# Kernel tuning notes

Hardware: AMD Instinct MI355X
Metric: run time of the kernel (lower is better)

Reference implementation:

```python
import jax, jax.numpy as jnp
import numpy as np
import math

B, S, HID = 1, 2048, 4096
HQ, HKV, D = 32, 8, 128
G = HQ // HKV          # GQA group size
OBS, W, SINK = 128, 32, 2
THETA = 500000.0
TOP_FRAC, MID_SPARSITY, LOW_FRAC = 0.05, 0.7, 0.20
K_KEEP = int(math.ceil((1.0 - MID_SPARSITY) * D))  # elements kept per level-1 token


def _rope(x):
    # x: [B, H, S, D]; standard Llama rotary embedding
    half = D // 2
    inv_freq = 1.0 / (THETA ** (jnp.arange(half, dtype=jnp.float32) / half))
    ang = jnp.arange(S, dtype=jnp.float32)[:, None] * inv_freq[None, :]  # [S, half]
    cos = jnp.concatenate([jnp.cos(ang), jnp.cos(ang)], axis=-1)  # [S, D]
    sin = jnp.concatenate([jnp.sin(ang), jnp.sin(ang)], axis=-1)
    x1, x2 = x[..., :half], x[..., half:]
    rot = jnp.concatenate([-x2, x1], axis=-1)
    return x * cos[None, None] + rot * sin[None, None]


def _topk_mask(x):
    # keep the K_KEEP largest-magnitude elements of each length-D token vector
    a = jnp.abs(x)
    thr = jnp.sort(a, axis=-1)[..., D - K_KEEP]
    return a >= thr[..., None]


def setup_inputs() -> dict:
    key = jax.random.key(0)
    ks = jax.random.split(key, 5)
    sc = HID ** -0.5
    return {
        "hidden_states": jax.random.normal(ks[0], (B, S, HID), dtype=jnp.float32),
        "wq": jax.random.normal(ks[1], (HID, HQ * D), dtype=jnp.float32) * sc,
        "wk": jax.random.normal(ks[2], (HID, HKV * D), dtype=jnp.float32) * sc,
        "wv": jax.random.normal(ks[3], (HID, HKV * D), dtype=jnp.float32) * sc,
        "wo": jax.random.normal(ks[4], (HQ * D, HID), dtype=jnp.float32) * sc,
    }


def reference(hidden_states, wq, wk, wv, wo):
    scale = 1.0 / math.sqrt(D)
    q = (hidden_states @ wq).reshape(B, S, HQ, D).transpose(0, 2, 1, 3)   # [B,HQ,S,D]
    k = (hidden_states @ wk).reshape(B, S, HKV, D).transpose(0, 2, 1, 3)  # [B,HKV,S,D]
    v = (hidden_states @ wv).reshape(B, S, HKV, D).transpose(0, 2, 1, 3)
    q, k = _rope(q), _rope(k)

    # --- observation-window GQA attention (grouped queries vs all keys) ---
    obs_q = q[:, :, S - OBS:, :].reshape(B, HKV, G, OBS, D)
    s_obs = jnp.einsum('bhgqd,bhkd->bhgqk', obs_q, k) * scale
    obs_causal = jnp.arange(S)[None, :] <= (S - OBS + jnp.arange(OBS))[:, None]  # [OBS,S]
    s_obs = jnp.where(obs_causal[None, None, None], s_obs, -jnp.inf)
    aw_kv = jax.nn.softmax(s_obs.astype(jnp.float32), axis=-1).mean(axis=2)  # [B,HKV,OBS,S]

    # per-token importance, normalized by how many obs queries observed each key
    counts = jnp.minimum(OBS, S - jnp.arange(S)).astype(jnp.float32)
    imp = aw_kv.sum(axis=2) / counts[None, None, :]  # [B,HKV,S]

    # --- global thresholds over the compressible region -> 3 sparsity levels ---
    imp_c = imp[:, :, :S - W].reshape(-1)
    t_high = jnp.quantile(imp_c, 1.0 - TOP_FRAC)
    t_low = jnp.quantile(imp_c, LOW_FRAC)
    level = jnp.where(imp >= t_high, 0, jnp.where(imp < t_low, 2, 1))
    pos = jnp.arange(S)
    dense_pos = (pos >= S - W) | (pos < SINK)     # recent window + sinks stay dense
    level = jnp.where(dense_pos[None, None, :], 0, level)

    keep_k = jnp.where((level == 0)[..., None], True, (level == 1)[..., None] & _topk_mask(k))
    keep_v = jnp.where((level == 0)[..., None], True, (level == 1)[..., None] & _topk_mask(v))
    k_sp = k * keep_k
    v_sp = v * keep_v
    evicted = level == 2

    # --- causal GQA attention over the sparsified KV cache ---
    q_g = q.reshape(B, HKV, G, S, D)
    s = jnp.einsum('bhgqd,bhkd->bhgqk', q_g, k_sp) * scale
    causal = jnp.tril(jnp.ones((S, S), dtype=bool))
    allow = causal[None, None, None] & (~evicted)[:, :, None, None, :]
    s = jnp.where(allow, s, -jnp.inf)
    p = jax.nn.softmax(s.astype(jnp.float32), axis=-1).astype(v_sp.dtype)
    o = jnp.einsum('bhgqk,bhkd->bhgqd', p, v_sp)
    o = o.reshape(B, HQ, S, D).transpose(0, 2, 1, 3).reshape(B, S, HQ * D)
    return o @ wo
```

## Files before the change

kernel.cpp:

```cpp
#include <hip/hip_runtime.h>
#include <hip/hip_bf16.h>
#include <math.h>

#define S_    2048
#define HID_  4096
#define HQ_   32
#define HKV_  8
#define D_    128
#define G_    4
#define OBS_  128
#define W_    32
#define NKV_  1024
#define NQ_   4096
#define KLD_  2048
#define SCALE_ 0.08838834764831845f
#define THR_IDX_ 89
#define NC_   16128

typedef __attribute__((ext_vector_type(4))) float f32x4;
typedef __attribute__((ext_vector_type(8))) short s16x8;
typedef __attribute__((ext_vector_type(8))) unsigned short u16x8;
typedef __attribute__((ext_vector_type(4))) unsigned short u16x4;
typedef unsigned short ushort_t;

struct TermPtrs { const ushort_t* a[6]; const ushort_t* b[6]; };
struct Six { const ushort_t* A[3]; const ushort_t* B[3]; };

__device__ __forceinline__ unsigned short f2bf(float x) {
  union { float f; unsigned u; } v; v.f = x;
  unsigned r = v.u + 0x7FFFu + ((v.u >> 16) & 1u);
  return (unsigned short)(r >> 16);
}
__device__ __forceinline__ float bf2f(unsigned short b) {
  union { unsigned u; float f; } v; v.u = ((unsigned)b) << 16;
  return v.f;
}
__device__ __forceinline__ void gload_lds16(const void* g, void* l) {
  __builtin_amdgcn_global_load_lds((const __attribute__((address_space(1))) unsigned int*)g,
                                   (__attribute__((address_space(3))) unsigned int*)l, 16, 0, 0);
}
__device__ __forceinline__ void term_sel(const TermPtrs& P, int tt,
                                         const ushort_t*& As, const ushort_t*& Bs) {
  switch (tt) {
    case 0: As = P.a[0]; Bs = P.b[0]; break;
    case 1: As = P.a[1]; Bs = P.b[1]; break;
    case 2: As = P.a[2]; Bs = P.b[2]; break;
    case 3: As = P.a[3]; Bs = P.b[3]; break;
    case 4: As = P.a[4]; Bs = P.b[4]; break;
    default: As = P.a[5]; Bs = P.b[5]; break;
  }
}
__device__ __forceinline__ void xcd_bmbn(int& bm, int& bn) {
  int nplane = gridDim.x * gridDim.y;
  int l = blockIdx.y * gridDim.x + blockIdx.x;
  int v = (l & 7) * (nplane >> 3) + (l >> 3);
  bm = v / gridDim.x;
  bn = v - bm * gridDim.x;
}

__global__ __launch_bounds__(256) void split3_kernel(const float* __restrict__ src,
                                                     ushort_t* __restrict__ d0,
                                                     ushort_t* __restrict__ d1,
                                                     ushort_t* __restrict__ d2, int n4) {
  int idx = blockIdx.x * 256 + threadIdx.x;
  if (idx >= n4) return;
  float4 v = ((const float4*)src)[idx];
  u16x4 o0, o1, o2;
  float xs[4] = {v.x, v.y, v.z, v.w};
#pragma unroll
  for (int e = 0; e < 4; ++e) {
    float x = xs[e];
    unsigned short b0 = f2bf(x);
    float r = x - bf2f(b0);
    unsigned short b1 = f2bf(r);
    o0[e] = b0; o1[e] = b1; o2[e] = f2bf(r - bf2f(b1));
  }
  *(u16x4*)(d0 + (size_t)idx * 4) = o0;
  *(u16x4*)(d1 + (size_t)idx * 4) = o1;
  *(u16x4*)(d2 + (size_t)idx * 4) = o2;
}

__global__ __launch_bounds__(256) void splitT_kernel(const float* __restrict__ src, int N,
                                                     ushort_t* __restrict__ t0,
                                                     ushort_t* __restrict__ t1,
                                                     ushort_t* __restrict__ t2) {
  __shared__ float tile[64][65];
  const int t = threadIdx.x;
  const int n0 = blockIdx.x * 64, k0 = blockIdx.y * 64;
#pragma unroll
  for (int i = 0; i < 16; ++i) {
    int idx = i * 256 + t;
    int r = idx >> 6, c = idx & 63;
    tile[r][c] = src[(size_t)(k0 + r) * N + n0 + c];
  }
  __syncthreads();
#pragma unroll
  for (int i = 0; i < 16; ++i) {
    int idx = i * 256 + t;
    int n = idx >> 6, kk = idx & 63;
    float x = tile[kk][n];
    unsigned short b0 = f2bf(x);
    size_t o = (size_t)(n0 + n) * HID_ + k0 + kk;
    t0[o] = b0;
    if (t1) {
      float r = x - bf2f(b0);
      unsigned short b1 = f2bf(r);
      t1[o] = b1;
      t2[o] = f2bf(r - bf2f(b1));
    }
  }
}

__global__ __launch_bounds__(256) void gemm6s(Six P, float* __restrict__ Cbase,
                                              int M, int N, int K, int KSTEPS) {
  __shared__ ushort_t lds[6 * 128 * 32];
  const int t = threadIdx.x;
  const int wave = t >> 6, lane = t & 63;
  const int lc = lane & 15, lg = lane >> 4;
  int bm, bn;
  xcd_bmbn(bm, bn);
  const int z = blockIdx.z;
  const int wm = wave >> 1, wn = wave & 1;
  float* C = Cbase + (size_t)z * M * N;

  f32x4 acc[4][4];
#pragma unroll
  for (int fi = 0; fi < 4; ++fi)
#pragma unroll
    for (int fj = 0; fj < 4; ++fj) acc[fi][fj] = 0.f;

  for (int kb = z * KSTEPS; kb < z * KSTEPS + KSTEPS; ++kb) {
    __syncthreads();
#pragma unroll
    for (int ti = 0; ti < 6; ++ti) {
      const ushort_t* src = (ti < 3) ? P.A[ti] : P.B[ti - 3];
      const int rb = ((ti < 3) ? bm : bn) * 128;
#pragma unroll
      for (int it = 0; it < 2; ++it) {
        int slot = it * 256 + t;
        int row = slot >> 2, cp = slot & 3;
        int c = (cp - (row >> 1)) & 3;
        gload_lds16(src + (size_t)(rb + row) * K + kb * 32 + c * 8,
                    lds + ti * 4096 + it * 2048 + wave * 512);
      }
    }
    __syncthreads();
    s16x8 a0[4], a1[4], a2[4], bfr[4];
#pragma unroll
    for (int f = 0; f < 4; ++f) {
      int ra = wm * 64 + f * 16 + lc;
      int ca = ((lg + (ra >> 1)) & 3) * 8;
      a0[f] = *(const s16x8*)(lds + 0 * 4096 + ra * 32 + ca);
      a1[f] = *(const s16x8*)(lds + 1 * 4096 + ra * 32 + ca);
      a2[f] = *(const s16x8*)(lds + 2 * 4096 + ra * 32 + ca);
    }
#pragma unroll
    for (int f = 0; f < 4; ++f) {
      int rb2 = wn * 64 + f * 16 + lc;
      bfr[f] = *(const s16x8*)(lds + 3 * 4096 + rb2 * 32 + (((lg + (rb2 >> 1)) & 3) * 8));
    }
#pragma unroll
    for (int fi = 0; fi < 4; ++fi)
#pragma unroll
      for (int fj = 0; fj < 4; ++fj) {
        acc[fi][fj] = __builtin_amdgcn_mfma_f32_16x16x32_bf16(a0[fi], bfr[fj], acc[fi][fj], 0, 0, 0);
        acc[fi][fj] = __builtin_amdgcn_mfma_f32_16x16x32_bf16(a1[fi], bfr[fj], acc[fi][fj], 0, 0, 0);
        acc[fi][fj] = __builtin_amdgcn_mfma_f32_16x16x32_bf16(a2[fi], bfr[fj], acc[fi][fj], 0, 0, 0);
      }
#pragma unroll
    for (int f = 0; f < 4; ++f) {
      int rb2 = wn * 64 + f * 16 + lc;
      bfr[f] = *(const s16x8*)(lds + 4 * 4096 + rb2 * 32 + (((lg + (rb2 >> 1)) & 3) * 8));
    }
#pragma unroll
    for (int fi = 0; fi < 4; ++fi)
#pragma unroll
      for (int fj = 0; fj < 4; ++fj) {
        acc[fi][fj] = __builtin_amdgcn_mfma_f32_16x16x32_bf16(a0[fi], bfr[fj], acc[fi][fj], 0, 0, 0);
        acc[fi][fj] = __builtin_amdgcn_mfma_f32_16x16x32_bf16(a1[fi], bfr[fj], acc[fi][fj], 0, 0, 0);
      }
#pragma unroll
    for (int f = 0; f < 4; ++f) {
      int rb2 = wn * 64 + f * 16 + lc;
      bfr[f] = *(const s16x8*)(lds + 5 * 4096 + rb2 * 32 + (((lg + (rb2 >> 1)) & 3) * 8));
    }
#pragma unroll
    for (int fi = 0; fi < 4; ++fi)
#pragma unroll
      for (int fj = 0; fj < 4; ++fj)
        acc[fi][fj] = __builtin_amdgcn_mfma_f32_16x16x32_bf16(a0[fi], bfr[fj], acc[fi][fj], 0, 0, 0);
  }
#pragma unroll
  for (int fi = 0; fi < 4; ++fi)
#pragma unroll
    for (int fj = 0; fj < 4; ++fj)
#pragma unroll
      for (int r = 0; r < 4; ++r)
        C[(size_t)(bm * 128 + wm * 64 + fi * 16 + lg * 4 + r) * N +
          bn * 128 + wn * 64 + fj * 16 + lc] = acc[fi][fj][r];
}

__global__ __launch_bounds__(256) void gemm1(const ushort_t* __restrict__ A,
                                             const ushort_t* __restrict__ B,
                                             float* __restrict__ Cbase,
                                             int M, int N, int K, int KSTEPS) {
  __shared__ ushort_t lds[2 * 128 * 64];
  const int t = threadIdx.x;
  const int wave = t >> 6, lane = t & 63;
  const int lc = lane & 15, lg = lane >> 4;
  int bm, bn;
  xcd_bmbn(bm, bn);
  const int z = blockIdx.z;
  const int wm = wave >> 1, wn = wave & 1;
  const int srow = t >> 3, schunk = t & 7;
  float* C = Cbase + (size_t)z * M * N;

  f32x4 acc[4][4];
#pragma unroll
  for (int fi = 0; fi < 4; ++fi)
#pragma unroll
    for (int fj = 0; fj < 4; ++fj) acc[fi][fj] = 0.f;

  for (int kb = z * KSTEPS; kb < z * KSTEPS + KSTEPS; ++kb) {
    __syncthreads();
#pragma unroll
    for (int g = 0; g < 4; ++g) {
      int row = g * 32 + srow;
      int sw = schunk ^ (row & 7);
      size_t co = kb * 64 + sw * 8;
      gload_lds16(A + (size_t)(bm * 128 + row) * K + co, lds + g * 2048 + wave * 512);
      gload_lds16(B + (size_t)(bn * 128 + row) * K + co, lds + 8192 + g * 2048 + wave * 512);
    }
    __syncthreads();
#pragma unroll
    for (int ks = 0; ks < 2; ++ks) {
      s16x8 af[4], bf[4];
#pragma unroll
      for (int f = 0; f < 4; ++f) {
        int ra = wm * 64 + f * 16 + lc;
        af[f] = *(const s16x8*)(lds + ra * 64 + (((ks * 4 + lg) ^ (ra & 7)) * 8));
        int rb = wn * 64 + f * 16 + lc;
        bf[f] = *(const s16x8*)(lds + 8192 + rb * 64 + (((ks * 4 + lg) ^ (rb & 7)) * 8));
      }
#pragma unroll
      for (int fi = 0; fi < 4; ++fi)
#pragma unroll
        for (int fj = 0; fj < 4; ++fj)
          acc[fi][fj] = __builtin_amdgcn_mfma_f32_16x16x32_bf16(af[fi], bf[fj], acc[fi][fj], 0, 0, 0);
    }
  }
#pragma unroll
  for (int fi = 0; fi < 4; ++fi)
#pragma unroll
    for (int fj = 0; fj < 4; ++fj)
#pragma unroll
      for (int r = 0; r < 4; ++r)
        C[(size_t)(bm * 128 + wm * 64 + fi * 16 + lg * 4 + r) * N +
          bn * 128 + wn * 64 + fj * 16 + lc] = acc[fi][fj][r];
}

__global__ __launch_bounds__(256) void gemm6z(TermPtrs P, float* __restrict__ Cg) {
  __shared__ ushort_t lds[2 * 128 * 64];
  const int t = threadIdx.x;
  const int wave = t >> 6, lane = t & 63;
  const int lc = lane & 15, lg = lane >> 4;
  const int bm = blockIdx.y, bn = blockIdx.x, z = blockIdx.z;
  const int wm = wave >> 1, wn = wave & 1;
  const int srow = t >> 3, schunk = t & 7;
  const size_t Aoff = (size_t)z * 512 * 128;
  const size_t Boff = (size_t)z * 2048 * 128;
  float* C = Cg + (size_t)z * 512 * 2048;

  f32x4 acc[4][4];
#pragma unroll
  for (int fi = 0; fi < 4; ++fi)
#pragma unroll
    for (int fj = 0; fj < 4; ++fj) acc[fi][fj] = 0.f;

  for (int tt = 0; tt < 6; ++tt) {
    const ushort_t *As, *Bs;
    term_sel(P, tt, As, Bs);
    As += Aoff; Bs += Boff;
    for (int kb = 0; kb < 2; ++kb) {
      __syncthreads();
#pragma unroll
      for (int g = 0; g < 4; ++g) {
        int row = g * 32 + srow;
        int sw = schunk ^ (row & 7);
        gload_lds16(As + (size_t)(bm * 128 + row) * 128 + kb * 64 + sw * 8,
                    lds + g * 2048 + wave * 512);
        gload_lds16(Bs + (size_t)(bn * 128 + row) * 128 + kb * 64 + sw * 8,
                    lds + 8192 + g * 2048 + wave * 512);
      }
      __syncthreads();
#pragma unroll
      for (int ks = 0; ks < 2; ++ks) {
        s16x8 af[4], bf[4];
#pragma unroll
        for (int f = 0; f < 4; ++f) {
          int ra = wm * 64 + f * 16 + lc;
          af[f] = *(const s16x8*)(lds + ra * 64 + (((ks * 4 + lg) ^ (ra & 7)) * 8));
          int rb = wn * 64 + f * 16 + lc;
          bf[f] = *(const s16x8*)(lds + 8192 + rb * 64 + (((ks * 4 + lg) ^ (rb & 7)) * 8));
        }
#pragma unroll
        for (int fi = 0; fi < 4; ++fi)
#pragma unroll
          for (int fj = 0; fj < 4; ++fj)
            acc[fi][fj] = __builtin_amdgcn_mfma_f32_16x16x32_bf16(af[fi], bf[fj], acc[fi][fj], 0, 0, 0);
      }
    }
  }
#pragma unroll
  for (int fi = 0; fi < 4; ++fi)
#pragma unroll
    for (int fj = 0; fj < 4; ++fj)
#pragma unroll
      for (int r = 0; r < 4; ++r)
        C[(size_t)(bm * 128 + wm * 64 + fi * 16 + lg * 4 + r) * 2048 +
          bn * 128 + wn * 64 + fj * 16 + lc] = acc[fi][fj][r];
}

__global__ __launch_bounds__(256) void kv_finish(const float* __restrict__ kvp,
                                                 const float* __restrict__ invf,
                                                 float* __restrict__ kvf,
                                                 ushort_t* __restrict__ k0,
                                                 ushort_t* __restrict__ k1,
                                                 ushort_t* __restrict__ k2) {
  const size_t n = (size_t)S_ * KLD_;
  int b = blockIdx.x;
  if (b < 4096) {
    int idx = b * 256 + threadIdx.x;
    int j = idx & 63;
    int h = (idx >> 6) & 7;
    int s = idx >> 9;
    size_t base = (size_t)s * KLD_ + h * 128 + j;
    float x1 = kvp[base] + kvp[base + n] + kvp[base + 2 * n] + kvp[base + 3 * n];
    float x2 = kvp[base + 64] + kvp[base + 64 + n] + kvp[base + 64 + 2 * n] + kvp[base + 64 + 3 * n];
    float ang = (float)s * invf[j];
    float sn, cs; sincosf(ang, &sn, &cs);
    float o1 = x1 * cs - x2 * sn;
    float o2 = x2 * cs + x1 * sn;
    kvf[base] = o1; kvf[base + 64] = o2;
    size_t o = (size_t)h * 262144 + (size_t)s * 128 + j;
    float ys[2] = {o1, o2};
#pragma unroll
    for (int e = 0; e < 2; ++e) {
      float x = ys[e];
      unsigned short b0 = f2bf(x);
      float r = x - bf2f(b0);
      unsigned short b1 = f2bf(r);
      k0[o + e * 64] = b0; k1[o + e * 64] = b1; k2[o + e * 64] = f2bf(r - bf2f(b1));
    }
  } else {
    int idx = (b - 4096) * 256 + threadIdx.x;
    int s = idx >> 8, c4 = idx & 255;
    size_t base = (size_t)s * KLD_ + 1024 + c4 * 4;
    float4 a = *(const float4*)(kvp + base);
    float4 bb = *(const float4*)(kvp + base + n);
    float4 c = *(const float4*)(kvp + base + 2 * n);
    float4 d = *(const float4*)(kvp + base + 3 * n);
    float4 o;
    o.x = a.x + bb.x + c.x + d.x; o.y = a.y + bb.y + c.y + d.y;
    o.z = a.z + bb.z + c.z + d.z; o.w = a.w + bb.w + c.w + d.w;
    *(float4*)(kvf + base) = o;
  }
}

__global__ void reduce2_kernel(const float* __restrict__ p, float* __restrict__ out, int n4) {
  int idx = blockIdx.x * 256 + threadIdx.x;
  if (idx >= n4) return;
  const size_t n = (size_t)n4 * 4;
  float4 a = ((const float4*)p)[idx];
  float4 b = ((const float4*)(p + n))[idx];
  float4 o;
  o.x = a.x + b.x; o.y = a.y + b.y; o.z = a.z + b.z; o.w = a.w + b.w;
  ((float4*)out)[idx] = o;
}

__global__ void freq_kernel(float* __restrict__ invf) {
  int j = threadIdx.x;
  if (j < 64) invf[j] = (float)(1.0 / pow(500000.0, (double)j / 64.0));
}

__global__ __launch_bounds__(256) void qobs_fuse(const float* __restrict__ qpart,
                                                 const float* __restrict__ invf,
                                                 ushort_t* __restrict__ q0,
                                                 ushort_t* __restrict__ q1,
                                                 ushort_t* __restrict__ q2) {
  int idx = blockIdx.x * 256 + threadIdx.x;
  int j = idx & 63;
  int hq = (idx >> 6) & 31;
  int i = idx >> 11;
  size_t base = (size_t)i * NQ_ + hq * 128 + j;
  float x1 = 0.f, x2 = 0.f;
#pragma unroll
  for (int z = 0; z < 8; ++z) {
    x1 += qpart[(size_t)z * OBS_ * NQ_ + base];
    x2 += qpart[(size_t)z * OBS_ * NQ_ + base + 64];
  }
  float ang = (float)(S_ - OBS_ + i) * invf[j];
  float sn, cs; sincosf(ang, &sn, &cs);
  float o1 = x1 * cs - x2 * sn;
  float o2 = x2 * cs + x1 * sn;
  int hk = hq >> 2, g = hq & 3;
  size_t o = (size_t)hk * 65536 + (size_t)(g * 128 + i) * 128 + j;
  float ys[2] = {o1, o2};
#pragma unroll
  for (int e = 0; e < 2; ++e) {
    float x = ys[e];
    unsigned short b0 = f2bf(x);
    float r = x - bf2f(b0);
    unsigned short b1 = f2bf(r);
    q0[o + e * 64] = b0; q1[o + e * 64] = b1; q2[o + e * 64] = f2bf(r - bf2f(b1));
  }
}

__global__ __launch_bounds__(256) void rope_q_fuse(const float* __restrict__ qp,
                                                   const float* __restrict__ invf,
                                                   ushort_t* __restrict__ qb16) {
  int idx = blockIdx.x * 256 + threadIdx.x;
  int j = idx & 63;
  int h = (idx >> 6) & 31;
  int s = idx >> 11;
  size_t base = (size_t)s * NQ_ + h * 128 + j;
  const size_t zs = (size_t)S_ * NQ_;
  float x1 = qp[base] + qp[base + zs];
  float x2 = qp[base + 64] + qp[base + 64 + zs];
  float ang = (float)s * invf[j];
  float sn, cs; sincosf(ang, &sn, &cs);
  qb16[base] = f2bf(x1 * cs - x2 * sn);
  qb16[base + 64] = f2bf(x2 * cs + x1 * sn);
}

__global__ __launch_bounds__(256) void rowstat_kernel(const float* __restrict__ s,
                                                      float* __restrict__ mx,
                                                      float* __restrict__ dinv) {
  const int row = blockIdx.x * 4 + (threadIdx.x >> 6);
  const int lane = threadIdx.x & 63;
  const int i = row & 127;
  const int jmax = S_ - OBS_ + i;
  const float* sp = s + (size_t)row * S_;
  float vals[32];
  float m = -INFINITY;
#pragma unroll
  for (int c = 0; c < 8; ++c) {
    int j0 = c * 256 + lane * 4;
    float4 v = *(const float4*)(sp + j0);
    float e0 = (j0 + 0 <= jmax) ? v.x * SCALE_ : -INFINITY;
    float e1 = (j0 + 1 <= jmax) ? v.y * SCALE_ : -INFINITY;
    float e2 = (j0 + 2 <= jmax) ? v.z * SCALE_ : -INFINITY;
    float e3 = (j0 + 3 <= jmax) ? v.w * SCALE_ : -INFINITY;
    vals[c * 4 + 0] = e0; vals[c * 4 + 1] = e1; vals[c * 4 + 2] = e2; vals[c * 4 + 3] = e3;
    m = fmaxf(m, fmaxf(fmaxf(e0, e1), fmaxf(e2, e3)));
  }
#pragma unroll
  for (int off = 1; off < 64; off <<= 1) m = fmaxf(m, __shfl_xor(m, off, 64));
  float ssum = 0.f;
#pragma unroll
  for (int c = 0; c < 32; ++c) ssum += expf(vals[c] - m);
#pragma unroll
  for (int off = 1; off < 64; off <<= 1) ssum += __shfl_xor(ssum, off, 64);
  if (lane == 0) { mx[row] = m; dinv[row] = 1.0f / ssum; }
}

__global__ __launch_bounds__(256) void colsum_part(const float* __restrict__ s,
                                                   const float* __restrict__ mx,
                                                   const float* __restrict__ dinv,
                                                   float* __restrict__ part) {
  __shared__ float mxl[64], dvl[64];
  const int jt = blockIdx.x, hk = blockIdx.y, rc = blockIdx.z;
  const int t = threadIdx.x;
  if (t < 64) {
    mxl[t] = mx[hk * 512 + rc * 64 + t];
    dvl[t] = dinv[hk * 512 + rc * 64 + t];
  }
  __syncthreads();
  const int j = jt * 256 + t;
  const float* sp = s + ((size_t)hk * 512 + rc * 64) * S_ + j;
  float acc = 0.f;
  for (int rr = 0; rr < 64; ++rr) {
    int i = (rc * 64 + rr) & 127;
    if (j <= S_ - OBS_ + i)
      acc += expf(sp[(size_t)rr * S_] * SCALE_ - mxl[rr]) * dvl[rr];
  }
  part[((size_t)rc * 8 + hk) * S_ + j] = acc;
}

__global__ void colsum_fin(const float* __restrict__ part, float* __restrict__ imp) {
  int idx = blockIdx.x * 256 + threadIdx.x;
  int hk = idx >> 11, j = idx & 2047;
  float acc = 0.f;
#pragma unroll
  for (int rc = 0; rc < 8; ++rc) acc += part[((size_t)rc * 8 + hk) * S_ + j];
  float cnt = (float)min(OBS_, S_ - j);
  imp[idx] = acc * 0.25f / cnt;
}

__global__ __launch_bounds__(1024) void radix_all(const float* __restrict__ imp,
                                                  float* __restrict__ thr) {
  __shared__ unsigned hist[4][256];
  __shared__ unsigned pfx_s[4], need_s[4];
  const int t = threadIdx.x;
  if (t < 4) {
    pfx_s[t] = 0u;
    need_s[t] = (t == 0) ? 3225u : (t == 1) ? 3226u : (t == 2) ? 15320u : 15321u;
  }
  __syncthreads();
  for (int pass = 0; pass < 4; ++pass) {
    ((unsigned*)hist)[t] = 0u;
    __syncthreads();
    int shift = 24 - pass * 8;
    for (int idx = t; idx < NC_; idx += 1024) {
      int h = idx / (S_ - W_), j = idx - h * (S_ - W_);
      union { float f; unsigned u; } cv; cv.f = imp[h * S_ + j];
      unsigned u = cv.u;
#pragma unroll
      for (int q = 0; q < 4; ++q) {
        bool m = (pass == 0) || ((u >> (shift + 8)) == (pfx_s[q] >> (shift + 8)));
        if (m) atomicAdd(&hist[q][(u >> shift) & 255u], 1u);
      }
    }
    __syncthreads();
    if (t < 4) {
      unsigned need = need_s[t], cum = 0, pfx = pfx_s[t];
      for (int d = 0; d < 256; ++d) {
        unsigned c = hist[t][d];
        if (cum + c > need) { pfx |= ((unsigned)d) << shift; need_s[t] = need - cum; break; }
        cum += c;
      }
      pfx_s[t] = pfx;
    }
    __syncthreads();
  }
  if (t == 0) {
    union { unsigned u; float f; } c0, c1, c2, c3;
    c0.u = pfx_s[0]; c1.u = pfx_s[1]; c2.u = pfx_s[2]; c3.u = pfx_s[3];
    double fl = 0.2 * (double)(NC_ - 1) - 3225.0;
    double fh = 0.95 * (double)(NC_ - 1) - 15320.0;
    thr[0] = (float)((double)c2.f + ((double)c3.f - (double)c2.f) * fh);
    thr[1] = (float)((double)c0.f + ((double)c1.f - (double)c0.f) * fl);
  }
}

__global__ __launch_bounds__(128) void sparsify_kernel(const float* __restrict__ kv,
                                                       const float* __restrict__ imp,
                                                       const float* __restrict__ thr,
                                                       ushort_t* __restrict__ ksp,
                                                       ushort_t* __restrict__ vsp,
                                                       float* __restrict__ ebias) {
  const int b = blockIdx.x;
  const int j = b >> 3;
  const int h = b & 7;
  const int t = threadIdx.x;
  float ipv = imp[h * S_ + j];
  bool dense = (j >= S_ - W_) || (j < 2);
  int lvl = dense ? 0 : ((ipv >= thr[0]) ? 0 : ((ipv < thr[1]) ? 2 : 1));
  if (t == 0) ebias[h * S_ + j] = (lvl == 2) ? -INFINITY : 0.0f;
  __shared__ float av[128];
  __shared__ float thv;
  size_t base_in = (size_t)j * KLD_ + h * D_;
  size_t base_out = (size_t)j * NKV_ + h * D_;
  float kvv = kv[base_in + t];
  av[t] = fabsf(kvv);
  __syncthreads();
  {
    float at = av[t]; int cnt = 0;
    for (int m = 0; m < 128; ++m) { float am = av[m]; cnt += (am < at) || (am == at && m < t); }
    if (cnt == THR_IDX_) thv = at;
  }
  __syncthreads();
  {
    bool keep = (lvl == 0) || (lvl == 1 && fabsf(kvv) >= thv);
    ksp[base_out + t] = f2bf(keep ? kvv : 0.0f);
  }
  __syncthreads();
  float vvv = kv[base_in + 1024 + t];
  av[t] = fabsf(vvv);
  __syncthreads();
  {
    float at = av[t]; int cnt = 0;
// ... 45 lines not shown
  const int h = xcd * 4 + (idx >> 4);
  const int p = idx & 15;
  const int hk = h >> 2;
  const int t = threadIdx.x;
  const int w = t >> 6, lane = t & 63;
  const int lc = lane & 15, lg = lane >> 4;

  const ushort_t* kbase = ksp + hk * D_;
  const ushort_t* vbase = vspT + (size_t)hk * D_ * S_;

  for (int strip = 0; strip < 2; ++strip) {
    const int qb = (strip == 0) ? p : 31 - p;
    const int q0 = qb * 64 + w * 16;
    s16x8 qfrag[4];
#pragma unroll
    for (int db = 0; db < 4; ++db)
      qfrag[db] = *(const s16x8*)(qbp + (size_t)(q0 + lc) * NQ_ + h * D_ + db * 32 + lg * 8);

    f32x4 o[8];
#pragma unroll
    for (int n = 0; n < 8; ++n) o[n] = 0.f;
    float mr[4] = {-INFINITY, -INFINITY, -INFINITY, -INFINITY};
    float lr[4] = {0.f, 0.f, 0.f, 0.f};

    const int ntj = qb + 1;
    for (int tj = 0; tj < ntj; ++tj) {
      const int j0 = tj * 64;
      __syncthreads();
#pragma unroll
      for (int i = 0; i < 4; ++i) {
        int slot = i * 256 + w * 64 + lane;
        int row = slot >> 4, c = slot & 15;
        const ushort_t* gp = kbase + (size_t)(j0 + row) * NKV_ + ((c ^ (row & 7)) * 8);
        gload_lds16(gp, &k_lds[(i * 256 + w * 64) * 8]);
      }
#pragma unroll
      for (int i = 0; i < 4; ++i) {
        int slot = i * 256 + w * 64 + lane;
        int d = slot >> 3, c = slot & 7;
        const ushort_t* gp = vbase + (size_t)d * S_ + j0 + ((c ^ (d & 7)) * 8);
        gload_lds16(gp, &vT_lds[(i * 256 + w * 64) * 8]);
      }
      __syncthreads();

      f32x4 sfr[4];
#pragma unroll
      for (int js = 0; js < 4; ++js) sfr[js] = 0.f;
#pragma unroll
      for (int js = 0; js < 4; ++js) {
        int row = js * 16 + lc;
#pragma unroll
        for (int db = 0; db < 4; ++db) {
          s16x8 kf = *(const s16x8*)&k_lds[row * 128 + (((db * 4 + lg) ^ (lc & 7)) * 8)];
          sfr[js] = __builtin_amdgcn_mfma_f32_16x16x32_bf16(qfrag[db], kf, sfr[js], 0, 0, 0);
        }
      }
      float eb[4];
#pragma unroll
      for (int js = 0; js < 4; ++js) eb[js] = ebias[hk * S_ + j0 + js * 16 + lc];

      const bool diag = (tj == qb);
      float sclv[4];
#pragma unroll
      for (int r = 0; r < 4; ++r) {
        float sv[4];
#pragma unroll
        for (int js = 0; js < 4; ++js) sv[js] = sfr[js][r] * SCALE_ + eb[js];
        if (diag) {
          int qrow = w * 16 + lg * 4 + r;
#pragma unroll
          for (int js = 0; js < 4; ++js)
            if (js * 16 + lc > qrow) sv[js] = -INFINITY;
        }
        float tm = fmaxf(fmaxf(sv[0], sv[1]), fmaxf(sv[2], sv[3]));
#pragma unroll
        for (int off = 1; off < 16; off <<= 1) tm = fmaxf(tm, __shfl_xor(tm, off, 64));
        float mnew = fmaxf(mr[r], tm);
        float scl = __expf(mr[r] - mnew);
        float ps = 0.f;
#pragma unroll
        for (int js = 0; js < 4; ++js) {
          float e = __expf(sv[js] - mnew);
          s_lds[w][lg * 4 + r][js * 16 + lc] = e;
          ps += e;
        }
#pragma unroll
        for (int off = 1; off < 16; off <<= 1) ps += __shfl_xor(ps, off, 64);
        lr[r] = lr[r] * scl + ps;
        mr[r] = mnew;
        sclv[r] = scl;
      }
#pragma unroll
      for (int n = 0; n < 8; ++n) {
        f32x4 ov = o[n];
#pragma unroll
        for (int r = 0; r < 4; ++r) ov[r] *= sclv[r];
        o[n] = ov;
      }
      asm volatile("s_waitcnt lgkmcnt(0)" ::: "memory");
      s16x8 pa[2];
#pragma unroll
      for (int ks = 0; ks < 2; ++ks) {
        float pv[8];
        *(f32x4*)&pv[0] = *(const f32x4*)&s_lds[w][lc][ks * 32 + lg * 8];
        *(f32x4*)&pv[4] = *(const f32x4*)&s_lds[w][lc][ks * 32 + lg * 8 + 4];
        s16x8 pk;
#pragma unroll
        for (int e = 0; e < 8; ++e) pk[e] = (short)f2bf(pv[e]);
        pa[ks] = pk;
      }
#pragma unroll
      for (int n = 0; n < 8; ++n) {
        int d = n * 16 + lc;
#pragma unroll
        for (int ks = 0; ks < 2; ++ks) {
          s16x8 vf = *(const s16x8*)&vT_lds[d * 64 + (((ks * 4 + lg) ^ (lc & 7)) * 8)];
          o[n] = __builtin_amdgcn_mfma_f32_16x16x32_bf16(pa[ks], vf, o[n], 0, 0, 0);
        }
      }
    }
#pragma unroll
    for (int r = 0; r < 4; ++r) {
      float rinv = 1.0f / lr[r];
      int row = q0 + lg * 4 + r;
#pragma unroll
      for (int n = 0; n < 8; ++n)
        ob16[(size_t)row * NQ_ + h * D_ + n * 16 + lc] = f2bf(o[n][r] * rinv);
    }
  }
}

extern "C" void kernel_launch(void* const* d_in, const int* in_sizes, int n_in,
                              void* d_out, int out_size, void* d_ws, size_t ws_size,
                              hipStream_t stream) {
  (void)in_sizes; (void)n_in; (void)out_size; (void)ws_size;
  const float* hid = (const float*)d_in[0];
  const float* wq  = (const float*)d_in[1];
  const float* wk  = (const float*)d_in[2];
  const float* wv  = (const float*)d_in[3];
  const float* wo  = (const float*)d_in[4];
  float* out = (float*)d_out;
  char* ws = (char*)d_ws;
  const size_t MB = 1ull << 20;

  ushort_t* h0     = (ushort_t*)(ws + 0 * MB);
  ushort_t* h1     = (ushort_t*)(ws + 16 * MB);
  ushort_t* h2     = (ushort_t*)(ws + 32 * MB);
  ushort_t* wq0T   = (ushort_t*)(ws + 48 * MB);
  ushort_t* wq1T   = (ushort_t*)(ws + 80 * MB);
  ushort_t* wq2T   = (ushort_t*)(ws + 112 * MB);
  ushort_t* wkv0T  = (ushort_t*)(ws + 144 * MB);
  ushort_t* wkv1T  = (ushort_t*)(ws + 160 * MB);
  ushort_t* wkv2T  = (ushort_t*)(ws + 176 * MB);
  float*    qpart  = (float*)(ws + 192 * MB);
  float*    kvf    = (float*)(ws + 192 * MB);
  float*    kvp    = (float*)(ws + 80 * MB);
  float*    qp2    = (float*)(ws + 80 * MB);
  ushort_t* qb16   = (ushort_t*)(ws + 16 * MB);
  ushort_t* kb0    = (ushort_t*)(ws + 32 * MB);
  ushort_t* kb1    = (ushort_t*)(ws + 36 * MB);
  ushort_t* kb2    = (ushort_t*)(ws + 40 * MB);
  float*    s_obs  = (float*)(ws + 48 * MB);
  ushort_t* woT    = (ushort_t*)(ws + 144 * MB);
  ushort_t* ksp    = (ushort_t*)(ws + 176 * MB);
  ushort_t* vsp    = (ushort_t*)(ws + 180 * MB);
  ushort_t* vspT   = (ushort_t*)(ws + 184 * MB);
  ushort_t* ob16   = (ushort_t*)(ws + 188 * MB + 512 * 1024);
  float*    opart  = (float*)(ws + 0 * MB);
  ushort_t* qo0    = (ushort_t*)(ws + 208 * MB);
  ushort_t* qo1    = (ushort_t*)(ws + 209 * MB);
  ushort_t* qo2    = (ushort_t*)(ws + 210 * MB);
  char*     misc   = ws + 212 * MB;
  float*    impv   = (float*)(misc + 0);
  float*    eb     = (float*)(misc + 64 * 1024);
  float*    invf   = (float*)(misc + 128 * 1024);
  float*    thr    = (float*)(misc + 132 * 1024);
  float*    mxbuf  = (float*)(misc + 160 * 1024);
  float*    dinvb  = (float*)(misc + 192 * 1024);
  float*    part   = (float*)(misc + 256 * 1024);

  freq_kernel<<<1, 64, 0, stream>>>(invf);

  split3_kernel<<<(S_ * HID_ / 4 + 255) / 256, 256, 0, stream>>>(hid, h0, h1, h2, S_ * HID_ / 4);
  splitT_kernel<<<dim3(NQ_ / 64, HID_ / 64), 256, 0, stream>>>(wq, NQ_, wq0T, wq1T, wq2T);
  splitT_kernel<<<dim3(NKV_ / 64, HID_ / 64), 256, 0, stream>>>(wk, NKV_, wkv0T, wkv1T, wkv2T);
  splitT_kernel<<<dim3(NKV_ / 64, HID_ / 64), 256, 0, stream>>>(
      wv, NKV_, wkv0T + (size_t)NKV_ * HID_, wkv1T + (size_t)NKV_ * HID_, wkv2T + (size_t)NKV_ * HID_);

  const size_t obs_off = (size_t)(S_ - OBS_) * HID_;
  {
    Six P;
    P.A[0] = h0 + obs_off; P.A[1] = h1 + obs_off; P.A[2] = h2 + obs_off;
    P.B[0] = wq0T; P.B[1] = wq1T; P.B[2] = wq2T;
    gemm6s<<<dim3(NQ_ / 128, 1, 8), 256, 0, stream>>>(P, qpart, 128, NQ_, HID_, 16);
  }
  qobs_fuse<<<(OBS_ * HQ_ * 64) / 256, 256, 0, stream>>>(qpart, invf, qo0, qo1, qo2);

  {
    Six P;
    P.A[0] = h0; P.A[1] = h1; P.A[2] = h2;
    P.B[0] = wkv0T; P.B[1] = wkv1T; P.B[2] = wkv2T;
    gemm6s<<<dim3(KLD_ / 128, S_ / 128, 4), 256, 0, stream>>>(P, kvp, S_, KLD_, HID_, 32);
  }
  kv_finish<<<6144, 256, 0, stream>>>(kvp, invf, kvf, kb0, kb1, kb2);

  gemm1<<<dim3(NQ_ / 128, S_ / 128, 2), 256, 0, stream>>>(h0, wq0T, qp2, S_, NQ_, HID_, 32);

  splitT_kernel<<<dim3(HID_ / 64, HID_ / 64), 256, 0, stream>>>(wo, HID_, woT, nullptr, nullptr);

  rope_q_fuse<<<(S_ * HQ_ * 64) / 256, 256, 0, stream>>>(qp2, invf, qb16);

  {
    TermPtrs P;
    P.a[0] = qo0; P.b[0] = kb0;
    P.a[1] = qo0; P.b[1] = kb1;
    P.a[2] = qo1; P.b[2] = kb0;
    P.a[3] = qo1; P.b[3] = kb1;
    P.a[4] = qo0; P.b[4] = kb2;
    P.a[5] = qo2; P.b[5] = kb0;
    gemm6z<<<dim3(16, 4, 8), 256, 0, stream>>>(P, s_obs);
  }
  rowstat_kernel<<<1024, 256, 0, stream>>>(s_obs, mxbuf, dinvb);
  colsum_part<<<dim3(8, 8, 8), 256, 0, stream>>>(s_obs, mxbuf, dinvb, part);
  colsum_fin<<<64, 256, 0, stream>>>(part, impv);

  radix_all<<<1, 1024, 0, stream>>>(impv, thr);

  sparsify_kernel<<<S_ * HKV_, 128, 0, stream>>>(kvf, impv, thr, ksp, vsp, eb);
  vtrans_kernel<<<dim3(S_ / 64, HKV_), 256, 0, stream>>>(vsp, vspT);
  attn_kernel<<<512, 256, 0, stream>>>(qb16, ksp, vspT, eb, ob16);
  gemm1<<<dim3(HID_ / 128, S_ / 128, 2), 256, 0, stream>>>(ob16, woT, opart, S_, HID_, HID_, 32);
  reduce2_kernel<<<(S_ * HID_ / 4 + 255) / 256, 256, 0, stream>>>(opart, out, S_ * HID_ / 4);
}
```

Baseline: 847.3 us.

## Merge prep kernels and co-schedule GEMMs with epilogues to cut launches and split-K

The four split/transpose launches and the frequency table are folded into one prep kernel. The observation-window Q GEMM and the KV GEMM now share a single launch. The full Q GEMM drops split-K and runs in the same launch as the KV RoPE finish, the q_obs finish and the wo transpose. The output projection also drops split-K and writes directly to the output, which removes the partial buffers and the reduce kernel. This trades fewer launches and less partial-sum traffic for heterogeneous blocks within a launch and lower parallelism per GEMM, and the KV partials are now staged in the output buffer.

```diff
diff --git a/kernel.cpp b/kernel.cpp
--- a/kernel.cpp
+++ b/kernel.cpp
@@ -24,7 +24,8 @@
 typedef unsigned short ushort_t;
 
 struct TermPtrs { const ushort_t* a[6]; const ushort_t* b[6]; };
-struct Six { const ushort_t* A[3]; const ushort_t* B[3]; };
+struct M1A { const ushort_t* A[3]; const ushort_t* B[3];
+             const ushort_t* QA[3]; const ushort_t* QB[3]; };
 
 __device__ __forceinline__ unsigned short f2bf(float x) {
   union { float f; unsigned u; } v; v.f = x;
@@ -58,46 +59,25 @@
   bn = v - bm * gridDim.x;
 }
 
-__global__ __launch_bounds__(256) void split3_kernel(const float* __restrict__ src,
-                                                     ushort_t* __restrict__ d0,
-                                                     ushort_t* __restrict__ d1,
-                                                     ushort_t* __restrict__ d2, int n4) {
-  int idx = blockIdx.x * 256 + threadIdx.x;
-  if (idx >= n4) return;
-  float4 v = ((const float4*)src)[idx];
-  u16x4 o0, o1, o2;
-  float xs[4] = {v.x, v.y, v.z, v.w};
-#pragma unroll
-  for (int e = 0; e < 4; ++e) {
-    float x = xs[e];
-    unsigned short b0 = f2bf(x);
-    float r = x - bf2f(b0);
-    unsigned short b1 = f2bf(r);
-    o0[e] = b0; o1[e] = b1; o2[e] = f2bf(r - bf2f(b1));
-  }
-  *(u16x4*)(d0 + (size_t)idx * 4) = o0;
-  *(u16x4*)(d1 + (size_t)idx * 4) = o1;
-  *(u16x4*)(d2 + (size_t)idx * 4) = o2;
-}
-
-__global__ __launch_bounds__(256) void splitT_kernel(const float* __restrict__ src, int N,
-                                                     ushort_t* __restrict__ t0,
-                                                     ushort_t* __restrict__ t1,
-                                                     ushort_t* __restrict__ t2) {
-  __shared__ float tile[64][65];
-  const int t = threadIdx.x;
-  const int n0 = blockIdx.x * 64, k0 = blockIdx.y * 64;
+__device__ __forceinline__ void splitT_body(const float* __restrict__ src, int N,
+                                            ushort_t* __restrict__ t0,
+                                            ushort_t* __restrict__ t1,
+                                            ushort_t* __restrict__ t2,
+                                            int idx, float (*tile)[65]) {
+  const int t = threadIdx.x;
+  const int ntx = N >> 6;
+  const int n0 = (idx % ntx) * 64, k0 = (idx / ntx) * 64;
 #pragma unroll
   for (int i = 0; i < 16; ++i) {
-    int idx = i * 256 + t;
-    int r = idx >> 6, c = idx & 63;
+    int s = i * 256 + t;
+    int r = s >> 6, c = s & 63;
     tile[r][c] = src[(size_t)(k0 + r) * N + n0 + c];
   }
   __syncthreads();
 #pragma unroll
   for (int i = 0; i < 16; ++i) {
-    int idx = i * 256 + t;
-    int n = idx >> 6, kk = idx & 63;
+    int s = i * 256 + t;
+    int n = s >> 6, kk = s & 63;
     float x = tile[kk][n];
     unsigned short b0 = f2bf(x);
     size_t o = (size_t)(n0 + n) * HID_ + k0 + kk;
@@ -111,17 +91,76 @@
   }
 }
 
-__global__ __launch_bounds__(256) void gemm6s(Six P, float* __restrict__ Cbase,
-                                              int M, int N, int K, int KSTEPS) {
+__global__ __launch_bounds__(256) void prep_kernel(const float* __restrict__ hid,
+                                                   const float* __restrict__ wq,
+                                                   const float* __restrict__ wk,
+                                                   const float* __restrict__ wv,
+                                                   ushort_t* h0, ushort_t* h1, ushort_t* h2,
+                                                   ushort_t* wq0T, ushort_t* wq1T, ushort_t* wq2T,
+                                                   ushort_t* wkv0T, ushort_t* wkv1T, ushort_t* wkv2T,
+                                                   float* invf) {
+  __shared__ float tile[64][65];
+  const int b = blockIdx.x;
+  if (b < 8192) {
+    int idx = b * 256 + threadIdx.x;
+    float4 v = ((const float4*)hid)[idx];
+    u16x4 o0, o1, o2;
+    float xs[4] = {v.x, v.y, v.z, v.w};
+#pragma unroll
+    for (int e = 0; e < 4; ++e) {
+      float x = xs[e];
+      unsigned short b0 = f2bf(x);
+      float r = x - bf2f(b0);
+      unsigned short b1 = f2bf(r);
+      o0[e] = b0; o1[e] = b1; o2[e] = f2bf(r - bf2f(b1));
+    }
+    *(u16x4*)(h0 + (size_t)idx * 4) = o0;
+    *(u16x4*)(h1 + (size_t)idx * 4) = o1;
+    *(u16x4*)(h2 + (size_t)idx * 4) = o2;
+  } else if (b < 12288) {
+    splitT_body(wq, NQ_, wq0T, wq1T, wq2T, b - 8192, tile);
+  } else if (b < 13312) {
+    splitT_body(wk, NKV_, wkv0T, wkv1T, wkv2T, b - 12288, tile);
+  } else if (b < 14336) {
+    splitT_body(wv, NKV_, wkv0T + (size_t)NKV_ * HID_, wkv1T + (size_t)NKV_ * HID_,
+                wkv2T + (size_t)NKV_ * HID_, b - 13312, tile);
+  } else {
+    int j = threadIdx.x;
+    if (j < 64) invf[j] = (float)(1.0 / pow(500000.0, (double)j / 64.0));
+  }
+}
+
+__global__ __launch_bounds__(256) void gemm6m(M1A P, float* __restrict__ kvp,
+                                              float* __restrict__ qpart) {
   __shared__ ushort_t lds[6 * 128 * 32];
   const int t = threadIdx.x;
   const int wave = t >> 6, lane = t & 63;
   const int lc = lane & 15, lg = lane >> 4;
-  int bm, bn;
-  xcd_bmbn(bm, bn);
+  const int wm = wave >> 1, wn = wave & 1;
   const int z = blockIdx.z;
-  const int wm = wave >> 1, wn = wave & 1;
-  float* C = Cbase + (size_t)z * M * N;
+
+  const ushort_t *As0, *As1, *As2, *Bs0, *Bs1, *Bs2;
+  float* C;
+  int rowA, rowB, kbeg, ksteps, N, crow0, ccol0;
+  if (z < 2) {
+    int bm, bn;
+    xcd_bmbn(bm, bn);
+    As0 = P.A[0]; As1 = P.A[1]; As2 = P.A[2];
+    Bs0 = P.B[0]; Bs1 = P.B[1]; Bs2 = P.B[2];
+    rowA = bm * 128; rowB = bn * 128;
+    kbeg = z * 64; ksteps = 64; N = KLD_;
+    C = kvp + (size_t)z * S_ * KLD_;
+    crow0 = bm * 128; ccol0 = bn * 128;
+  } else {
+    int l = blockIdx.y * gridDim.x + blockIdx.x;
+    int bn = l & 31, ks = l >> 5;
+    As0 = P.QA[0]; As1 = P.QA[1]; As2 = P.QA[2];
+    Bs0 = P.QB[0]; Bs1 = P.QB[1]; Bs2 = P.QB[2];
+    rowA = 0; rowB = bn * 128;
+    kbeg = ks * 16; ksteps = 16; N = NQ_;
+    C = qpart + (size_t)ks * 128 * NQ_;
+    crow0 = 0; ccol0 = bn * 128;
+  }
 
   f32x4 acc[4][4];
 #pragma unroll
@@ -129,18 +168,19 @@
 #pragma unroll
     for (int fj = 0; fj < 4; ++fj) acc[fi][fj] = 0.f;
 
-  for (int kb = z * KSTEPS; kb < z * KSTEPS + KSTEPS; ++kb) {
+  for (int kb = kbeg; kb < kbeg + ksteps; ++kb) {
     __syncthreads();
 #pragma unroll
     for (int ti = 0; ti < 6; ++ti) {
-      const ushort_t* src = (ti < 3) ? P.A[ti] : P.B[ti - 3];
-      const int rb = ((ti < 3) ? bm : bn) * 128;
+      const ushort_t* src = (ti == 0) ? As0 : (ti == 1) ? As1 : (ti == 2) ? As2
+                          : (ti == 3) ? Bs0 : (ti == 4) ? Bs1 : Bs2;
+      const int rb = (ti < 3) ? rowA : rowB;
 #pragma unroll
       for (int it = 0; it < 2; ++it) {
         int slot = it * 256 + t;
         int row = slot >> 2, cp = slot & 3;
         int c = (cp - (row >> 1)) & 3;
-        gload_lds16(src + (size_t)(rb + row) * K + kb * 32 + c * 8,
+        gload_lds16(src + (size_t)(rb + row) * HID_ + kb * 32 + c * 8,
                     lds + ti * 4096 + it * 2048 + wave * 512);
       }
     }
@@ -196,24 +236,21 @@
     for (int fj = 0; fj < 4; ++fj)
 #pragma unroll
       for (int r = 0; r < 4; ++r)
-        C[(size_t)(bm * 128 + wm * 64 + fi * 16 + lg * 4 + r) * N +
-          bn * 128 + wn * 64 + fj * 16 + lc] = acc[fi][fj][r];
-}
-
-__global__ __launch_bounds__(256) void gemm1(const ushort_t* __restrict__ A,
-                                             const ushort_t* __restrict__ B,
-                                             float* __restrict__ Cbase,
-                                             int M, int N, int K, int KSTEPS) {
-  __shared__ ushort_t lds[2 * 128 * 64];
+        C[(size_t)(crow0 + wm * 64 + fi * 16 + lg * 4 + r) * N +
+          ccol0 + wn * 64 + fj * 16 + lc] = acc[fi][fj][r];
+}
+
+__device__ __forceinline__ void gemm1_body(const ushort_t* __restrict__ A,
+                                           const ushort_t* __restrict__ B,
+                                           float* __restrict__ C,
+                                           int N, int K, int KSTEPS, ushort_t* lds) {
   const int t = threadIdx.x;
   const int wave = t >> 6, lane = t & 63;
   const int lc = lane & 15, lg = lane >> 4;
   int bm, bn;
   xcd_bmbn(bm, bn);
-  const int z = blockIdx.z;
   const int wm = wave >> 1, wn = wave & 1;
   const int srow = t >> 3, schunk = t & 7;
-  float* C = Cbase + (size_t)z * M * N;
 
   f32x4 acc[4][4];
 #pragma unroll
@@ -221,7 +258,7 @@
 #pragma unroll
     for (int fj = 0; fj < 4; ++fj) acc[fi][fj] = 0.f;
 
-  for (int kb = z * KSTEPS; kb < z * KSTEPS + KSTEPS; ++kb) {
+  for (int kb = 0; kb < KSTEPS; ++kb) {
     __syncthreads();
 #pragma unroll
     for (int g = 0; g < 4; ++g) {
@@ -257,6 +294,107 @@
       for (int r = 0; r < 4; ++r)
         C[(size_t)(bm * 128 + wm * 64 + fi * 16 + lg * 4 + r) * N +
           bn * 128 + wn * 64 + fj * 16 + lc] = acc[fi][fj][r];
+}
+
+__global__ __launch_bounds__(256) void gemm1(const ushort_t* __restrict__ A,
+                                             const ushort_t* __restrict__ B,
+                                             float* __restrict__ C,
+                                             int N, int K, int KSTEPS) {
+  __shared__ ushort_t lds[2 * 128 * 64];
+  gemm1_body(A, B, C, N, K, KSTEPS, lds);
+}
+
+__global__ __launch_bounds__(256) void m2_kernel(const ushort_t* __restrict__ h0,
+                                                 const ushort_t* __restrict__ wq0T,
+                                                 float* __restrict__ qf,
+                                                 const float* __restrict__ kvp,
+                                                 const float* __restrict__ invf,
+                                                 float* __restrict__ kvf,
+                                                 ushort_t* __restrict__ k0,
+                                                 ushort_t* __restrict__ k1,
+                                                 ushort_t* __restrict__ k2,
+                                                 const float* __restrict__ qpart,
+                                                 ushort_t* __restrict__ q0,
+                                                 ushort_t* __restrict__ q1,
+                                                 ushort_t* __restrict__ q2,
+                                                 const float* __restrict__ wo,
+                                                 ushort_t* __restrict__ woT) {
+  __shared__ ushort_t lds[2 * 128 * 64];
+  if (blockIdx.z == 0) {
+    gemm1_body(h0, wq0T, qf, NQ_, HID_, 64, lds);
+    return;
+  }
+  const int l = blockIdx.y * gridDim.x + blockIdx.x;
+  const int t = threadIdx.x;
+  const size_t n = (size_t)S_ * KLD_;
+  for (int vb = l; vb < 6144; vb += 512) {
+    if (vb < 4096) {
+      int idx = vb * 256 + t;
+      int j = idx & 63;
+      int h = (idx >> 6) & 7;
+      int s = idx >> 9;
+      size_t base = (size_t)s * KLD_ + h * 128 + j;
+      float x1 = kvp[base] + kvp[base + n];
+      float x2 = kvp[base + 64] + kvp[base + 64 + n];
+      float ang = (float)s * invf[j];
+      float sn, cs; sincosf(ang, &sn, &cs);
+      float o1 = x1 * cs - x2 * sn;
+      float o2 = x2 * cs + x1 * sn;
+      kvf[base] = o1; kvf[base + 64] = o2;
+      size_t o = (size_t)h * 262144 + (size_t)s * 128 + j;
+      float ys[2] = {o1, o2};
+#pragma unroll
+      for (int e = 0; e < 2; ++e) {
+        float x = ys[e];
+        unsigned short b0 = f2bf(x);
+        float r = x - bf2f(b0);
+        unsigned short b1 = f2bf(r);
+        k0[o + e * 64] = b0; k1[o + e * 64] = b1; k2[o + e * 64] = f2bf(r - bf2f(b1));
+      }
+    } else {
+      int idx = (vb - 4096) * 256 + t;
+      int s = idx >> 8, c4 = idx & 255;
+      size_t base = (size_t)s * KLD_ + 1024 + c4 * 4;
+      float4 a = *(const float4*)(kvp + base);
+      float4 bb = *(const float4*)(kvp + base + n);
+      float4 o;
+      o.x = a.x + bb.x; o.y = a.y + bb.y; o.z = a.z + bb.z; o.w = a.w + bb.w;
+      *(float4*)(kvf + base) = o;
+    }
+  }
+  for (int vb = l; vb < 1024; vb += 512) {
+    int idx = vb * 256 + t;
+    int j = idx & 63;
+    int hq = (idx >> 6) & 31;
+    int i = idx >> 11;
+    size_t base = (size_t)i * NQ_ + hq * 128 + j;
+    float x1 = 0.f, x2 = 0.f;
+#pragma unroll
+    for (int z = 0; z < 8; ++z) {
+      x1 += qpart[(size_t)z * OBS_ * NQ_ + base];
+      x2 += qpart[(size_t)z * OBS_ * NQ_ + base + 64];
+    }
+    float ang = (float)(S_ - OBS_ + i) * invf[j];
+    float sn, cs; sincosf(ang, &sn, &cs);
+    float o1 = x1 * cs - x2 * sn;
+    float o2 = x2 * cs + x1 * sn;
+    int hk = hq >> 2, g = hq & 3;
+    size_t o = (size_t)hk * 65536 + (size_t)(g * 128 + i) * 128 + j;
+    float ys[2] = {o1, o2};
+#pragma unroll
+    for (int e = 0; e < 2; ++e) {
+      float x = ys[e];
+      unsigned short b0 = f2bf(x);
+      float r = x - bf2f(b0);
+      unsigned short b1 = f2bf(r);
+      q0[o + e * 64] = b0; q1[o + e * 64] = b1; q2[o + e * 64] = f2bf(r - bf2f(b1));
+    }
+  }
+  float (*tile)[65] = (float(*)[65])lds;
+  for (int vb = l; vb < 4096; vb += 512) {
+    __syncthreads();
+    splitT_body(wo, HID_, woT, nullptr, nullptr, vb, tile);
+  }
 }
 
 __global__ __launch_bounds__(256) void gemm6z(TermPtrs P, float* __restrict__ Cg) {
@@ -321,102 +459,7 @@
           bn * 128 + wn * 64 + fj * 16 + lc] = acc[fi][fj][r];
 }
 
-__global__ __launch_bounds__(256) void kv_finish(const float* __restrict__ kvp,
-                                                 const float* __restrict__ invf,
-                                                 float* __restrict__ kvf,
-                                                 ushort_t* __restrict__ k0,
-                                                 ushort_t* __restrict__ k1,
-                                                 ushort_t* __restrict__ k2) {
-  const size_t n = (size_t)S_ * KLD_;
-  int b = blockIdx.x;
-  if (b < 4096) {
-    int idx = b * 256 + threadIdx.x;
-    int j = idx & 63;
-    int h = (idx >> 6) & 7;
-    int s = idx >> 9;
-    size_t base = (size_t)s * KLD_ + h * 128 + j;
-    float x1 = kvp[base] + kvp[base + n] + kvp[base + 2 * n] + kvp[base + 3 * n];
-    float x2 = kvp[base + 64] + kvp[base + 64 + n] + kvp[base + 64 + 2 * n] + kvp[base + 64 + 3 * n];
-    float ang = (float)s * invf[j];
-    float sn, cs; sincosf(ang, &sn, &cs);
-    float o1 = x1 * cs - x2 * sn;
-    float o2 = x2 * cs + x1 * sn;
-    kvf[base] = o1; kvf[base + 64] = o2;
-    size_t o = (size_t)h * 262144 + (size_t)s * 128 + j;
-    float ys[2] = {o1, o2};
-#pragma unroll
-    for (int e = 0; e < 2; ++e) {
-      float x = ys[e];
-      unsigned short b0 = f2bf(x);
-      float r = x - bf2f(b0);
-      unsigned short b1 = f2bf(r);
-      k0[o + e * 64] = b0; k1[o + e * 64] = b1; k2[o + e * 64] = f2bf(r - bf2f(b1));
-    }
-  } else {
-    int idx = (b - 4096) * 256 + threadIdx.x;
-    int s = idx >> 8, c4 = idx & 255;
-    size_t base = (size_t)s * KLD_ + 1024 + c4 * 4;
-    float4 a = *(const float4*)(kvp + base);
-    float4 bb = *(const float4*)(kvp + base + n);
-    float4 c = *(const float4*)(kvp + base + 2 * n);
-    float4 d = *(const float4*)(kvp + base + 3 * n);
-    float4 o;
-    o.x = a.x + bb.x + c.x + d.x; o.y = a.y + bb.y + c.y + d.y;
-    o.z = a.z + bb.z + c.z + d.z; o.w = a.w + bb.w + c.w + d.w;
-    *(float4*)(kvf + base) = o;
-  }
-}
-
-__global__ void reduce2_kernel(const float* __restrict__ p, float* __restrict__ out, int n4) {
-  int idx = blockIdx.x * 256 + threadIdx.x;
-  if (idx >= n4) return;
-  const size_t n = (size_t)n4 * 4;
-  float4 a = ((const float4*)p)[idx];
-  float4 b = ((const float4*)(p + n))[idx];
-  float4 o;
-  o.x = a.x + b.x; o.y = a.y + b.y; o.z = a.z + b.z; o.w = a.w + b.w;
-  ((float4*)out)[idx] = o;
-}
-
-__global__ void freq_kernel(float* __restrict__ invf) {
-  int j = threadIdx.x;
-  if (j < 64) invf[j] = (float)(1.0 / pow(500000.0, (double)j / 64.0));
-}
-
-__global__ __launch_bounds__(256) void qobs_fuse(const float* __restrict__ qpart,
-                                                 const float* __restrict__ invf,
-                                                 ushort_t* __restrict__ q0,
-                                                 ushort_t* __restrict__ q1,
-                                                 ushort_t* __restrict__ q2) {
-  int idx = blockIdx.x * 256 + threadIdx.x;
-  int j = idx & 63;
-  int hq = (idx >> 6) & 31;
-  int i = idx >> 11;
-  size_t base = (size_t)i * NQ_ + hq * 128 + j;
-  float x1 = 0.f, x2 = 0.f;
-#pragma unroll
-  for (int z = 0; z < 8; ++z) {
-    x1 += qpart[(size_t)z * OBS_ * NQ_ + base];
-    x2 += qpart[(size_t)z * OBS_ * NQ_ + base + 64];
-  }
-  float ang = (float)(S_ - OBS_ + i) * invf[j];
-  float sn, cs; sincosf(ang, &sn, &cs);
-  float o1 = x1 * cs - x2 * sn;
-  float o2 = x2 * cs + x1 * sn;
-  int hk = hq >> 2, g = hq & 3;
-  size_t o = (size_t)hk * 65536 + (size_t)(g * 128 + i) * 128 + j;
-  float ys[2] = {o1, o2};
-#pragma unroll
-  for (int e = 0; e < 2; ++e) {
-    float x = ys[e];
-    unsigned short b0 = f2bf(x);
-    float r = x - bf2f(b0);
-    unsigned short b1 = f2bf(r);
-    q0[o + e * 64] = b0; q1[o + e * 64] = b1; q2[o + e * 64] = f2bf(r - bf2f(b1));
-  }
-}
-
-__global__ __launch_bounds__(256) void rope_q_fuse(const float* __restrict__ qp,
+__global__ __launch_bounds__(256) void rope_q_fuse(const float* __restrict__ qf,
                                                    const float* __restrict__ invf,
                                                    ushort_t* __restrict__ qb16) {
   int idx = blockIdx.x * 256 + threadIdx.x;
@@ -424,9 +467,8 @@
   int h = (idx >> 6) & 31;
   int s = idx >> 11;
   size_t base = (size_t)s * NQ_ + h * 128 + j;
-  const size_t zs = (size_t)S_ * NQ_;
-  float x1 = qp[base] + qp[base + zs];
-  float x2 = qp[base + 64] + qp[base + 64 + zs];
+  float x1 = qf[base];
+  float x2 = qf[base + 64];
   float ang = (float)s * invf[j];
   float sn, cs; sincosf(ang, &sn, &cs);
   qb16[base] = f2bf(x1 * cs - x2 * sn);
@@ -778,10 +820,10 @@
   ushort_t* wkv0T  = (ushort_t*)(ws + 144 * MB);
   ushort_t* wkv1T  = (ushort_t*)(ws + 160 * MB);
   ushort_t* wkv2T  = (ushort_t*)(ws + 176 * MB);
+  float*    kvp    = (float*)d_out;
   float*    qpart  = (float*)(ws + 192 * MB);
-  float*    kvf    = (float*)(ws + 192 * MB);
-  float*    kvp    = (float*)(ws + 80 * MB);
-  float*    qp2    = (float*)(ws + 80 * MB);
+  float*    qf     = (float*)(ws + 80 * MB);
+  float*    kvf    = (float*)(ws + 112 * MB);
   ushort_t* qb16   = (ushort_t*)(ws + 16 * MB);
   ushort_t* kb0    = (ushort_t*)(ws + 32 * MB);
   ushort_t* kb1    = (ushort_t*)(ws + 36 * MB);
@@ -792,7 +834,6 @@
   ushort_t* vsp    = (ushort_t*)(ws + 180 * MB);
   ushort_t* vspT   = (ushort_t*)(ws + 184 * MB);
   ushort_t* ob16   = (ushort_t*)(ws + 188 * MB + 512 * 1024);
-  float*    opart  = (float*)(ws + 0 * MB);
   ushort_t* qo0    = (ushort_t*)(ws + 208 * MB);
   ushort_t* qo1    = (ushort_t*)(ws + 209 * MB);
   ushort_t* qo2    = (ushort_t*)(ws + 210 * MB);
@@ -805,36 +846,24 @@
   float*    dinvb  = (float*)(misc + 192 * 1024);
   float*    part   = (float*)(misc + 256 * 1024);
 
-  freq_kernel<<<1, 64, 0, stream>>>(invf);
-
-  split3_kernel<<<(S_ * HID_ / 4 + 255) / 256, 256, 0, stream>>>(hid, h0, h1, h2, S_ * HID_ / 4);
-  splitT_kernel<<<dim3(NQ_ / 64, HID_ / 64), 256, 0, stream>>>(wq, NQ_, wq0T, wq1T, wq2T);
-  splitT_kernel<<<dim3(NKV_ / 64, HID_ / 64), 256, 0, stream>>>(wk, NKV_, wkv0T, wkv1T, wkv2T);
-  splitT_kernel<<<dim3(NKV_ / 64, HID_ / 64), 256, 0, stream>>>(
-      wv, NKV_, wkv0T + (size_t)NKV_ * HID_, wkv1T + (size_t)NKV_ * HID_, wkv2T + (size_t)NKV_ * HID_);
+  prep_kernel<<<14337, 256, 0, stream>>>(hid, wq, wk, wv, h0, h1, h2,
+                                         wq0T, wq1T, wq2T, wkv0T, wkv1T, wkv2T, invf);
 
   const size_t obs_off = (size_t)(S_ - OBS_) * HID_;
   {
-    Six P;
-    P.A[0] = h0 + obs_off; P.A[1] = h1 + obs_off; P.A[2] = h2 + obs_off;
-    P.B[0] = wq0T; P.B[1] = wq1T; P.B[2] = wq2T;
-    gemm6s<<<dim3(NQ_ / 128, 1, 8), 256, 0, stream>>>(P, qpart, 128, NQ_, HID_, 16);
-  }
-  qobs_fuse<<<(OBS_ * HQ_ * 64) / 256, 256, 0, stream>>>(qpart, invf, qo0, qo1, qo2);
-
-  {
-    Six P;
+    M1A P;
     P.A[0] = h0; P.A[1] = h1; P.A[2] = h2;
     P.B[0] = wkv0T; P.B[1] = wkv1T; P.B[2] = wkv2T;
-    gemm6s<<<dim3(KLD_ / 128, S_ / 128, 4), 256, 0, stream>>>(P, kvp, S_, KLD_, HID_, 32);
-  }
-  kv_finish<<<6144, 256, 0, stream>>>(kvp, invf, kvf, kb0, kb1, kb2);
-
-  gemm1<<<dim3(NQ_ / 128, S_ / 128, 2), 256, 0, stream>>>(h0, wq0T, qp2, S_, NQ_, HID_, 32);
-
-  splitT_kernel<<<dim3(HID_ / 64, HID_ / 64), 256, 0, stream>>>(wo, HID_, woT, nullptr, nullptr);
-
-  rope_q_fuse<<<(S_ * HQ_ * 64) / 256, 256, 0, stream>>>(qp2, invf, qb16);
+    P.QA[0] = h0 + obs_off; P.QA[1] = h1 + obs_off; P.QA[2] = h2 + obs_off;
+    P.QB[0] = wq0T; P.QB[1] = wq1T; P.QB[2] = wq2T;
+    gemm6m<<<dim3(16, 16, 3), 256, 0, stream>>>(P, kvp, qpart);
+  }
+
+  m2_kernel<<<dim3(32, 16, 2), 256, 0, stream>>>(h0, wq0T, qf, kvp, invf, kvf,
+                                                 kb0, kb1, kb2, qpart, qo0, qo1, qo2,
+                                                 wo, woT);
+
+  rope_q_fuse<<<(S_ * HQ_ * 64) / 256, 256, 0, stream>>>(qf, invf, qb16);
 
   {
     TermPtrs P;
@@ -846,15 +875,15 @@
     P.a[5] = qo2; P.b[5] = kb0;
     gemm6z<<<dim3(16, 4, 8), 256, 0, stream>>>(P, s_obs);
   }
+
   rowstat_kernel<<<1024, 256, 0, stream>>>(s_obs, mxbuf, dinvb);
   colsum_part<<<dim3(8, 8, 8), 256, 0, stream>>>(s_obs, mxbuf, dinvb, part);
   colsum_fin<<<64, 256, 0, stream>>>(part, impv);
-
   radix_all<<<1, 1024, 0, stream>>>(impv, thr);
 
   sparsify_kernel<<<S_ * HKV_, 128, 0, stream>>>(kvf, impv, thr, ksp, vsp, eb);
   vtrans_kernel<<<dim3(S_ / 64, HKV_), 256, 0, stream>>>(vsp, vspT);
   attn_kernel<<<512, 256, 0, stream>>>(qb16, ksp, vspT, eb, ob16);
-  gemm1<<<dim3(HID_ / 128, S_ / 128, 2), 256, 0, stream>>>(ob16, woT, opart, S_, HID_, HID_, 32);
-  reduce2_kernel<<<(S_ * HID_ / 4 + 255) / 256, 256, 0, stream>>>(opart, out, S_ * HID_ / 4);
-}
+
+  gemm1<<<dim3(32, 16, 1), 256, 0, stream>>>(ob16, woT, out, HID_, HID_, 64);
+}
```

New measurement: 786.7 us. 1.08x faster.
